# Optimization experiments

Measured on AMD Instinct MI355X. Metric: run time of the kernel, lower is better.

The kernel has to match this reference:

```python
import jax, jax.numpy as jnp
import numpy as np

B, N, K, H = 8, 2048, 30, 128
SCALE = 30.0
EPS = 1e-5


def _gelu(x):
    return jax.nn.gelu(x, approximate=False)


def _lin(x, w, b):
    return x @ w.T + b


def _ln(x, g, b):
    m = x.mean(-1, keepdims=True)
    v = ((x - m) ** 2).mean(-1, keepdims=True)
    return g * (x - m) * jax.lax.rsqrt(v + EPS) + b


def _gather_nodes(h_V, E_idx):
    # h_V: [B,N,H], E_idx: [B,N,K] -> [B,N,K,H]
    b_idx = jnp.arange(h_V.shape[0])[:, None, None]
    return h_V[b_idx, E_idx]


def setup_inputs() -> dict:
    key = jax.random.key(0)
    ks = jax.random.split(key, 16)
    p = 0.02
    inp = {
        'h_V': jax.random.normal(ks[0], (B, N, H), jnp.float32),
        'h_E': jax.random.normal(ks[1], (B, N, K, H), jnp.float32),
        'E_idx': jax.random.randint(ks[2], (B, N, K), 0, N, jnp.int32),
        'mask_V': jnp.ones((B, N), jnp.float32),
        'mask_attend': jnp.ones((B, N, K), jnp.float32),
        # node message MLP (3H -> H -> H -> H)
        'W1_w': jax.random.normal(ks[3], (H, 3 * H), jnp.float32) * p,
        'W1_b': jnp.zeros((H,), jnp.float32),
        'W2_w': jax.random.normal(ks[4], (H, H), jnp.float32) * p,
        'W2_b': jnp.zeros((H,), jnp.float32),
        'W3_w': jax.random.normal(ks[5], (H, H), jnp.float32) * p,
        'W3_b': jnp.zeros((H,), jnp.float32),
        # edge message MLP (3H -> H -> H -> H)
        'W11_w': jax.random.normal(ks[6], (H, 3 * H), jnp.float32) * p,
        'W11_b': jnp.zeros((H,), jnp.float32),
        'W12_w': jax.random.normal(ks[7], (H, H), jnp.float32) * p,
        'W12_b': jnp.zeros((H,), jnp.float32),
        'W13_w': jax.random.normal(ks[8], (H, H), jnp.float32) * p,
        'W13_b': jnp.zeros((H,), jnp.float32),
        # layer norms
        'n1_g': jnp.ones((H,), jnp.float32), 'n1_b': jnp.zeros((H,), jnp.float32),
        'n2_g': jnp.ones((H,), jnp.float32), 'n2_b': jnp.zeros((H,), jnp.float32),
        'n3_g': jnp.ones((H,), jnp.float32), 'n3_b': jnp.zeros((H,), jnp.float32),
        # position-wise FFN (H -> 4H -> H)
        'din_w': jax.random.normal(ks[9], (4 * H, H), jnp.float32) * p,
        'din_b': jnp.zeros((4 * H,), jnp.float32),
        'dout_w': jax.random.normal(ks[10], (H, 4 * H), jnp.float32) * p,
        'dout_b': jnp.zeros((H,), jnp.float32),
    }
    return inp


def reference(h_V, h_E, E_idx, mask_V, mask_attend,
              W1_w, W1_b, W2_w, W2_b, W3_w, W3_b,
              W11_w, W11_b, W12_w, W12_b, W13_w, W13_b,
              n1_g, n1_b, n2_g, n2_b, n3_g, n3_b,
              din_w, din_b, dout_w, dout_b):
    k = h_E.shape[-2]
    # --- node update ---
    h_nbr = _gather_nodes(h_V, E_idx)                       # [B,N,K,H]
    h_V_exp = jnp.broadcast_to(h_V[:, :, None, :], h_nbr.shape)
    h_EV = jnp.concatenate([h_V_exp, h_nbr, h_E], axis=-1)  # [B,N,K,3H]
    h_message = _lin(_gelu(_lin(_gelu(_lin(h_EV, W1_w, W1_b)), W2_w, W2_b)), W3_w, W3_b)
    h_message = mask_attend[..., None] * h_message
    dh = jnp.sum(h_message, axis=-2) / SCALE
    h_V = _ln(h_V + dh, n1_g, n1_b)
    dh = _lin(_gelu(_lin(h_V, din_w, din_b)), dout_w, dout_b)
    h_V = _ln(h_V + dh, n2_g, n2_b)
    h_V = mask_V[..., None] * h_V
    # --- edge update ---
    h_nbr = _gather_nodes(h_V, E_idx)
    h_V_exp = jnp.broadcast_to(h_V[:, :, None, :], h_nbr.shape)
    h_EV = jnp.concatenate([h_V_exp, h_nbr, h_E], axis=-1)
    h_message = _lin(_gelu(_lin(_gelu(_lin(h_EV, W11_w, W11_b)), W12_w, W12_b)), W13_w, W13_b)
    h_E = _ln(h_E + h_message, n3_g, n3_b)
    return (h_V, h_E)
```

## Files before the change

### kernel.cpp

```cpp
#include <hip/hip_runtime.h>

#define B_ 8
#define N_ 2048
#define K_ 30
#define H_ 128
#define LDA 136
#define EPS_ 1e-5f

typedef __attribute__((ext_vector_type(8))) short short8;
typedef __attribute__((ext_vector_type(4))) float f32x4;

__device__ inline unsigned pkbf(float lo, float hi) {
  unsigned r;
  asm("v_cvt_pk_bf16_f32 %0, %1, %2" : "=v"(r) : "v"(lo), "v"(hi));
  return r;
}

__device__ inline unsigned short f2bf(float f) { return (unsigned short)pkbf(f, f); }

__device__ inline float bf2f(unsigned short h) {
  union { unsigned u; float f; } v; v.u = ((unsigned)h) << 16; return v.f;
}

__device__ inline float gelu_t(float x) {
  const float p = x * x;
  const float z = x * (1.5957691216057308f + 0.07135481627f * p);
  const float e = exp2f(z * -1.4426950408889634f);
  return x * __builtin_amdgcn_rcpf(1.0f + e);
}

__device__ inline short8 pack8(float4 a, float4 b) {
  union { unsigned u[4]; short8 s; } v;
  v.u[0] = pkbf(a.x, a.y); v.u[1] = pkbf(a.z, a.w);
  v.u[2] = pkbf(b.x, b.y); v.u[3] = pkbf(b.z, b.w);
  return v.s;
}

template<int LDW>
__device__ inline void gemmT(const unsigned short* __restrict__ sA,
                             const unsigned short* __restrict__ W,
                             int lane, int cb, f32x4 (&acc)[4][2]) {
  const int rl = lane & 15;
  const int klo = (lane >> 4) << 3;
#pragma unroll
  for (int ks = 0; ks < 4; ++ks) {
    short8 wf[2];
#pragma unroll
    for (int fn = 0; fn < 2; ++fn)
      wf[fn] = *(const short8*)(W + (size_t)(cb + fn * 16 + rl) * LDW + ks * 32 + klo);
#pragma unroll
    for (int et = 0; et < 4; ++et) {
      const short8 ef = *(const short8*)(sA + (et * 16 + rl) * LDA + ks * 32 + klo);
      acc[et][0] = __builtin_amdgcn_mfma_f32_16x16x32_bf16(wf[0], ef, acc[et][0], 0, 0, 0);
      acc[et][1] = __builtin_amdgcn_mfma_f32_16x16x32_bf16(wf[1], ef, acc[et][1], 0, 0, 0);
    }
  }
}

#define ZERO42(A) \
  _Pragma("unroll") for (int e_ = 0; e_ < 4; ++e_) { A[e_][0] = (f32x4){0,0,0,0}; A[e_][1] = (f32x4){0,0,0,0}; }

template<int LDW, int NN>
__device__ inline void gemm64(const unsigned short* __restrict__ sA,
                              const unsigned short* __restrict__ W,
                              int lane, int cb, f32x4 (&acc)[4][NN]) {
  const int rl = lane & 15;
  const int klo = (lane >> 4) << 3;
#pragma unroll
  for (int ks = 0; ks < 4; ++ks) {
    short8 a[4];
#pragma unroll
    for (int m = 0; m < 4; ++m)
      a[m] = *(const short8*)(sA + (m * 16 + rl) * LDA + ks * 32 + klo);
#pragma unroll
    for (int n = 0; n < NN; ++n) {
      const short8 b8 = *(const short8*)(W + (size_t)(cb + n * 16 + rl) * LDW + ks * 32 + klo);
#pragma unroll
      for (int m = 0; m < 4; ++m)
        acc[m][n] = __builtin_amdgcn_mfma_f32_16x16x32_bf16(a[m], b8, acc[m][n], 0, 0, 0);
    }
  }
}

__global__ __launch_bounds__(256) void prep(const float* __restrict__ w1, const float* __restrict__ w2,
                                            const float* __restrict__ w3, const float* __restrict__ w11,
                                            const float* __restrict__ w12, const float* __restrict__ w13,
                                            const float* __restrict__ din, const float* __restrict__ dout,
                                            unsigned short* __restrict__ dst) {
  const int i = blockIdx.x * 256 + threadIdx.x;
  const float* s; int off;
  if (i < 49152)       { s = w1;  off = 0; }
  else if (i < 65536)  { s = w2;  off = 49152; }
  else if (i < 81920)  { s = w3;  off = 65536; }
  else if (i < 131072) { s = w11; off = 81920; }
  else if (i < 147456) { s = w12; off = 131072; }
  else if (i < 163840) { s = w13; off = 147456; }
  else if (i < 229376) { s = din; off = 163840; }
  else                 { s = dout; off = 229376; }
  dst[i] = f2bf(s[i - off]);
}

template<bool F32SRC, bool SPLIT>
__global__ __launch_bounds__(256) void preY(const void* __restrict__ Xv,
                                            const unsigned short* __restrict__ Wbase,
                                            unsigned short* __restrict__ Yc,
                                            unsigned short* __restrict__ Yn) {
  __shared__ __align__(16) unsigned short sA[64 * LDA];
  const int tid = threadIdx.x;
  const int lane = tid & 63;
  const int w = tid >> 6;
  const int rows = blockIdx.x << 6;
  const int rl = lane & 15;
  const int h4 = (lane >> 4) << 2;

  if (F32SRC) {
    const float* X = (const float*)Xv;
    for (int t = tid; t < 1024; t += 256) {
      const int r = t >> 4, seg = t & 15;
      const float* src = X + (((size_t)(rows + r)) << 7) + seg * 8;
      *(short8*)(sA + r * LDA + seg * 8) = pack8(*(const float4*)src, *(const float4*)(src + 4));
    }
  } else {
    const unsigned short* X = (const unsigned short*)Xv;
    for (int t = tid; t < 1024; t += 256) {
      const int r = t >> 4, seg = t & 15;
      *(short8*)(sA + r * LDA + seg * 8) =
          *(const short8*)(X + (((size_t)(rows + r)) << 7) + seg * 8);
    }
  }
  __syncthreads();

  const int half = w >> 1;
  const int cb = (w & 1) * 64;
  f32x4 acc[4][4];
#pragma unroll
  for (int m = 0; m < 4; ++m)
#pragma unroll
    for (int n = 0; n < 4; ++n) acc[m][n] = (f32x4){0, 0, 0, 0};
  gemm64<384, 4>(sA, Wbase + half * 128, lane, cb, acc);

  unsigned short* Y = half ? Yn : Yc;
  const int stride = SPLIT ? 128 : 256;
  const int coff = SPLIT ? 0 : half * 128;
#pragma unroll
  for (int n = 0; n < 4; ++n) {
    const int col = coff + cb + n * 16 + rl;
#pragma unroll
    for (int m = 0; m < 4; ++m)
#pragma unroll
      for (int i = 0; i < 4; ++i)
        Y[(size_t)(rows + m * 16 + h4 + i) * stride + col] = f2bf(acc[m][n][i]);
  }
}

__global__ __launch_bounds__(256, 6) void k1(
    const float* __restrict__ hV, const float* __restrict__ hE,
    const int* __restrict__ Eidx, const float* __restrict__ mattend,
    const unsigned short* __restrict__ wc, const unsigned short* __restrict__ Y1,
    const float* __restrict__ W1b, const float* __restrict__ W2b,
    const float* __restrict__ W3b, const float* __restrict__ n1g,
    const float* __restrict__ n1b, unsigned short* __restrict__ hV1b) {
  __shared__ __align__(16) unsigned short sA[64 * LDA];
  __shared__ __align__(16) unsigned short sYc[2 * 128];
  __shared__ float sMask[64];
  __shared__ float sRed[2][128];

  const int tid = threadIdx.x;
  const int lane = tid & 63;
  const int w = tid >> 6;
  const int rl = lane & 15;
  const int h4 = (lane >> 4) << 2;
  const int bid = (blockIdx.x & 7) * 1024 + (blockIdx.x >> 3);
  const int v0 = bid << 1;
  const int b = v0 >> 11;
  const int n0 = v0 & (N_ - 1);
  const int bBase = b * N_;

  const unsigned short* W1c = wc;
  const unsigned short* W2c = wc + 49152;
  const unsigned short* W3c = wc + 65536;

  for (int t = tid; t < 1024; t += 256) {
    const int r = t >> 4, seg = t & 15;
    const int g = r >> 5;
    int kk = r & 31; if (kk >= K_) kk = K_ - 1;
    const size_t e = (size_t)(bBase + n0 + g) * K_ + kk;
    const float* src = hE + (e << 7) + seg * 8;
    *(short8*)(sA + r * LDA + seg * 8) = pack8(*(const float4*)src, *(const float4*)(src + 4));
  }
  {
    const int g = tid >> 7, c = tid & 127;
    sYc[g * 128 + c] = Y1[(size_t)(bBase + n0 + g) * 256 + c];
  }
  if (tid < 64) {
    const int g = tid >> 5, kk = tid & 31;
    sMask[tid] = (kk < K_) ? mattend[(bBase + n0 + g) * K_ + kk] : 0.f;
  }
  __syncthreads();

  f32x4 acc[4][2];
  ZERO42(acc)
  gemmT<384>(sA, W1c + 256, lane, w * 32, acc);
  __syncthreads();

  for (int t = tid; t < 1024; t += 256) {
    const int r = t >> 4, seg = t & 15;
    const int g = r >> 5;
    int kk = r & 31; if (kk >= K_) kk = K_ - 1;
    const int j = Eidx[(bBase + n0 + g) * K_ + kk];
    *(short8*)(sA + r * LDA + seg * 8) =
        *(const short8*)(Y1 + (size_t)(bBase + j) * 256 + 128 + seg * 8);
  }
  __syncthreads();

  {
    float4 b1v[2];
    b1v[0] = *(const float4*)(W1b + w * 32 + h4);
    b1v[1] = *(const float4*)(W1b + w * 32 + 16 + h4);
#pragma unroll
    for (int et = 0; et < 4; ++et) {
      const int e = et * 16 + rl;
      const int g = et >> 1;
#pragma unroll
      for (int fn = 0; fn < 2; ++fn) {
        const int f0 = w * 32 + fn * 16 + h4;
        const ushort4 yc = *(const ushort4*)(sYc + g * 128 + f0);
        const ushort4 yn = *(const ushort4*)(sA + e * LDA + f0);
        const float x0 = gelu_t(acc[et][fn][0] + b1v[fn].x + bf2f(yc.x) + bf2f(yn.x));
        const float x1 = gelu_t(acc[et][fn][1] + b1v[fn].y + bf2f(yc.y) + bf2f(yn.y));
        const float x2 = gelu_t(acc[et][fn][2] + b1v[fn].z + bf2f(yc.z) + bf2f(yn.z));
        const float x3 = gelu_t(acc[et][fn][3] + b1v[fn].w + bf2f(yc.w) + bf2f(yn.w));
        uint2 o; o.x = pkbf(x0, x1); o.y = pkbf(x2, x3);
        *(uint2*)(sA + e * LDA + f0) = o;
      }
    }
  }
  __syncthreads();

  f32x4 acc2[4][2];
  ZERO42(acc2)
  gemmT<128>(sA, W2c, lane, w * 32, acc2);
  __syncthreads();
  {
    float4 b2v[2];
    b2v[0] = *(const float4*)(W2b + w * 32 + h4);
    b2v[1] = *(const float4*)(W2b + w * 32 + 16 + h4);
#pragma unroll
    for (int et = 0; et < 4; ++et) {
      const int e = et * 16 + rl;
#pragma unroll
      for (int fn = 0; fn < 2; ++fn) {
        const int f0 = w * 32 + fn * 16 + h4;
        const float x0 = gelu_t(acc2[et][fn][0] + b2v[fn].x);
        const float x1 = gelu_t(acc2[et][fn][1] + b2v[fn].y);
        const float x2 = gelu_t(acc2[et][fn][2] + b2v[fn].z);
        const float x3 = gelu_t(acc2[et][fn][3] + b2v[fn].w);
        uint2 o; o.x = pkbf(x0, x1); o.y = pkbf(x2, x3);
        *(uint2*)(sA + e * LDA + f0) = o;
      }
    }
  }
  __syncthreads();

  f32x4 acc3[4][2];
  ZERO42(acc3)
  gemmT<128>(sA, W3c, lane, w * 32, acc3);
  __syncthreads();

  {
    float4 b3v[2];
    b3v[0] = *(const float4*)(W3b + w * 32 + h4);
    b3v[1] = *(const float4*)(W3b + w * 32 + 16 + h4);
#pragma unroll
    for (int et = 0; et < 4; ++et) {
      const int e = et * 16 + rl;
      const float mk = sMask[e];
#pragma unroll
      for (int fn = 0; fn < 2; ++fn) {
        const int f0 = w * 32 + fn * 16 + h4;
        uint2 o;
        o.x = pkbf((acc3[et][fn][0] + b3v[fn].x) * mk, (acc3[et][fn][1] + b3v[fn].y) * mk);
        o.y = pkbf((acc3[et][fn][2] + b3v[fn].z) * mk, (acc3[et][fn][3] + b3v[fn].w) * mk);
        *(uint2*)(sA + e * LDA + f0) = o;
      }
    }
  }
  __syncthreads();

  {
    const int g = tid >> 7, f = tid & 127;
    float s = 0.f;
#pragma unroll
    for (int kk = 0; kk < 32; ++kk) s += bf2f(sA[(g * 32 + kk) * LDA + f]);
    sRed[g][f] = s;
  }
  __syncthreads();

  if (w < 2) {
    const size_t base = ((size_t)(bBase + n0 + w)) << 7;
    const float x0 = hV[base + lane] + sRed[w][lane] * (1.0f / 30.0f);
    const float x1 = hV[base + 64 + lane] + sRed[w][64 + lane] * (1.0f / 30.0f);
    float s = x0 + x1;
#pragma unroll
    for (int o = 1; o < 64; o <<= 1) s += __shfl_xor(s, o);
    const float mean = s * (1.0f / 128.0f);
    const float d0 = x0 - mean, d1 = x1 - mean;
    float vs = d0 * d0 + d1 * d1;
#pragma unroll
    for (int o = 1; o < 64; o <<= 1) vs += __shfl_xor(vs, o);
    const float inv = rsqrtf(vs * (1.0f / 128.0f) + EPS_);
    hV1b[base + lane] = f2bf(n1g[lane] * (d0 * inv) + n1b[lane]);
    hV1b[base + 64 + lane] = f2bf(n1g[64 + lane] * (d1 * inv) + n1b[64 + lane]);
  }
}

__global__ __launch_bounds__(256) void k2(
    const unsigned short* __restrict__ hV1b, const unsigned short* __restrict__ wc,
    const float* __restrict__ dinb, const float* __restrict__ doutb,
    const float* __restrict__ n2g, const float* __restrict__ n2b,
    const float* __restrict__ maskV, float* __restrict__ outV,
    unsigned short* __restrict__ hV2c) {
  __shared__ __align__(16) unsigned short sT[16 * LDA];
  __shared__ float sStat[16][2][4];

  const int tid = threadIdx.x;
  const int lane = tid & 63;
  const int w = tid >> 6;
  const int rl = lane & 15;
  const int h4 = (lane >> 4) << 2;
  const int klo = (lane >> 4) << 3;
  const int rowbase = blockIdx.x << 4;

  const unsigned short* dinc = wc + 163840;
  const unsigned short* doutc = wc + 229376;

  short8 ef[4];
#pragma unroll
  for (int ks = 0; ks < 4; ++ks)
    ef[ks] = *(const short8*)(hV1b + (((size_t)(rowbase + rl)) << 7) + ks * 32 + klo);

  f32x4 acc2[2];
  acc2[0] = (f32x4){0, 0, 0, 0}; acc2[1] = (f32x4){0, 0, 0, 0};

  for (int c = 0; c < 4; ++c) {
    f32x4 acc1[2];
    acc1[0] = (f32x4){0, 0, 0, 0}; acc1[1] = (f32x4){0, 0, 0, 0};
#pragma unroll
    for (int ks = 0; ks < 4; ++ks)
#pragma unroll
      for (int fn = 0; fn < 2; ++fn) {
        const short8 wf = *(const short8*)(dinc + (size_t)(c * 128 + w * 32 + fn * 16 + rl) * 128 + ks * 32 + klo);
        acc1[fn] = __builtin_amdgcn_mfma_f32_16x16x32_bf16(wf, ef[ks], acc1[fn], 0, 0, 0);
      }
    __syncthreads();
    {
      float4 db[2];
      db[0] = *(const float4*)(dinb + c * 128 + w * 32 + h4);
      db[1] = *(const float4*)(dinb + c * 128 + w * 32 + 16 + h4);
#pragma unroll
      for (int fn = 0; fn < 2; ++fn) {
        const int f0 = w * 32 + fn * 16 + h4;
        const float x0 = gelu_t(acc1[fn][0] + db[fn].x);
        const float x1 = gelu_t(acc1[fn][1] + db[fn].y);
        const float x2 = gelu_t(acc1[fn][2] + db[fn].z);
        const float x3 = gelu_t(acc1[fn][3] + db[fn].w);
        uint2 o; o.x = pkbf(x0, x1); o.y = pkbf(x2, x3);
        *(uint2*)(sT + rl * LDA + f0) = o;
      }
    }
    __syncthreads();
#pragma unroll
    for (int ks = 0; ks < 4; ++ks) {
      const short8 xf = *(const short8*)(sT + rl * LDA + ks * 32 + klo);
#pragma unroll
      for (int fn = 0; fn < 2; ++fn) {
        const short8 wf2 = *(const short8*)(doutc + (size_t)(w * 32 + fn * 16 + rl) * 512 + c * 128 + ks * 32 + klo);
        acc2[fn] = __builtin_amdgcn_mfma_f32_16x16x32_bf16(wf2, xf, acc2[fn], 0, 0, 0);
      }
    }
  }

  const int row = rl;
  const int grow = rowbase + row;
  {
    float4 wbv[2];
    wbv[0] = *(const float4*)(doutb + w * 32 + h4);
    wbv[1] = *(const float4*)(doutb + w * 32 + 16 + h4);
    float s = 0.f, ss = 0.f;
#pragma unroll
    for (int fn = 0; fn < 2; ++fn) {
      const int f0 = w * 32 + fn * 16 + h4;
      const ushort4 rr = *(const ushort4*)(hV1b + (((size_t)grow) << 7) + f0);
      const float x0 = acc2[fn][0] + wbv[fn].x + bf2f(rr.x);
      const float x1 = acc2[fn][1] + wbv[fn].y + bf2f(rr.y);
      const float x2 = acc2[fn][2] + wbv[fn].z + bf2f(rr.z);
      const float x3 = acc2[fn][3] + wbv[fn].w + bf2f(rr.w);
      acc2[fn] = (f32x4){x0, x1, x2, x3};
      s += x0 + x1 + x2 + x3;
      ss += x0 * x0 + x1 * x1 + x2 * x2 + x3 * x3;
    }
    s += __shfl_xor(s, 16); s += __shfl_xor(s, 32);
    ss += __shfl_xor(ss, 16); ss += __shfl_xor(ss, 32);
    if (lane < 16) { sStat[row][0][w] = s; sStat[row][1][w] = ss; }
  }
  __syncthreads();
  {
    const float sum = sStat[row][0][0] + sStat[row][0][1] + sStat[row][0][2] + sStat[row][0][3];
    const float ssq = sStat[row][1][0] + sStat[row][1][1] + sStat[row][1][2] + sStat[row][1][3];
    const float mean = sum * (1.0f / 128.0f);
    const float inv = rsqrtf(ssq * (1.0f / 128.0f) - mean * mean + EPS_);
    const float mv = maskV[grow];
#pragma unroll
    for (int fn = 0; fn < 2; ++fn) {
      const int f0 = w * 32 + fn * 16 + h4;
      const float4 gv = *(const float4*)(n2g + f0);
      const float4 bv = *(const float4*)(n2b + f0);
      const float y0 = (gv.x * (acc2[fn][0] - mean) * inv + bv.x) * mv;
      const float y1 = (gv.y * (acc2[fn][1] - mean) * inv + bv.y) * mv;
      const float y2 = (gv.z * (acc2[fn][2] - mean) * inv + bv.z) * mv;
      const float y3 = (gv.w * (acc2[fn][3] - mean) * inv + bv.w) * mv;
      *(float4*)(outV + (((size_t)grow) << 7) + f0) = make_float4(y0, y1, y2, y3);
      uint2 o; o.x = pkbf(y0, y1); o.y = pkbf(y2, y3);
      *(uint2*)(hV2c + (((size_t)grow) << 7) + f0) = o;
    }
  }
}

__global__ __launch_bounds__(256, 6) void k3(
    const float* __restrict__ hE, const int* __restrict__ Eidx,
    const unsigned short* __restrict__ wc,
    const unsigned short* __restrict__ Y2c, const unsigned short* __restrict__ Y2n,
    const float* __restrict__ W11b, const float* __restrict__ W12b,
    const float* __restrict__ W13b, const float* __restrict__ n3g,
    const float* __restrict__ n3b, float* __restrict__ outE) {
  __shared__ __align__(16) unsigned short sA[64 * LDA];
  __shared__ unsigned short sYc[2 * 128];
  __shared__ float sStat[64][2][4];

  const int tid = threadIdx.x;
  const int lane = tid & 63;
  const int w = tid >> 6;
  const int rl = lane & 15;
  const int h4 = (lane >> 4) << 2;
  const int bid = (blockIdx.x & 7) * 1024 + (blockIdx.x >> 3);
  const int v0 = bid << 1;
  const int b = v0 >> 11;
  const int n0 = v0 & (N_ - 1);
  const int bBase = b * N_;

  const unsigned short* W11c = wc + 81920;
  const unsigned short* W12c = wc + 131072;
  const unsigned short* W13c = wc + 147456;

  for (int t = tid; t < 1024; t += 256) {
    const int r = t >> 4, seg = t & 15;
    const int g = r >> 5;
    int kk = r & 31; if (kk >= K_) kk = K_ - 1;
    const size_t e = (size_t)(bBase + n0 + g) * K_ + kk;
    const float* src = hE + (e << 7) + seg * 8;
    *(short8*)(sA + r * LDA + seg * 8) = pack8(*(const float4*)src, *(const float4*)(src + 4));
  }
  {
    const int g = tid >> 7, c = tid & 127;
    sYc[g * 128 + c] = Y2c[(size_t)(bBase + n0 + g) * 128 + c];
  }
  __syncthreads();

  f32x4 acc[4][2];
  ZERO42(acc)
  gemm64<384, 2>(sA, W11c + 256, lane, w * 32, acc);
  __syncthreads();

  for (int t = tid; t < 1024; t += 256) {
    const int r = t >> 4, seg = t & 15;
    const int g = r >> 5;
    int kk = r & 31; if (kk >= K_) kk = K_ - 1;
    const int j = Eidx[(bBase + n0 + g) * K_ + kk];
    *(short8*)(sA + r * LDA + seg * 8) =
        *(const short8*)(Y2n + (size_t)(bBase + j) * 128 + seg * 8);
  }
  __syncthreads();

#pragma unroll
  for (int n = 0; n < 2; ++n) {
    const int f = w * 32 + n * 16 + rl;
    const float bb = W11b[f];
#pragma unroll
    for (int m = 0; m < 4; ++m)
#pragma unroll
      for (int i = 0; i < 4; ++i) {
        const int e = m * 16 + h4 + i;
        const float x = acc[m][n][i] + bb + bf2f(sYc[(e >> 5) * 128 + f]) + bf2f(sA[e * LDA + f]);
        sA[e * LDA + f] = f2bf(gelu_t(x));
      }
  }
  __syncthreads();

  f32x4 acc2[4][2];
  ZERO42(acc2)
  gemm64<128, 2>(sA, W12c, lane, w * 32, acc2);
  __syncthreads();
#pragma unroll
  for (int n = 0; n < 2; ++n) {
    const int f = w * 32 + n * 16 + rl;
    const float bb = W12b[f];
#pragma unroll
    for (int m = 0; m < 4; ++m)
#pragma unroll
      for (int i = 0; i < 4; ++i) {
        const int e = m * 16 + h4 + i;
        sA[e * LDA + f] = f2bf(gelu_t(acc2[m][n][i] + bb));
      }
  }
  __syncthreads();

  f32x4 acc3[4][2];
  ZERO42(acc3)
  gemm64<128, 2>(sA, W13c, lane, w * 32, acc3);

  float gc[2], bc[2], wb[2];
#pragma unroll
  for (int n = 0; n < 2; ++n) {
    const int f = w * 32 + n * 16 + rl;
    gc[n] = n3g[f]; bc[n] = n3b[f]; wb[n] = W13b[f];
  }
#pragma unroll
  for (int m = 0; m < 4; ++m)
#pragma unroll
    for (int i = 0; i < 4; ++i) {
      const int e = m * 16 + h4 + i;
      const int g = e >> 5, kk = e & 31;
      const bool valid = kk < K_;
      const float* er = hE + (((size_t)((bBase + n0 + g) * K_ + (valid ? kk : K_ - 1))) << 7) + w * 32 + rl;
      float s = 0.f, ss = 0.f;
#pragma unroll
      for (int n = 0; n < 2; ++n) {
        float x = acc3[m][n][i] + wb[n];
        if (valid) x += er[n * 16];
        acc3[m][n][i] = x;
        s += x; ss += x * x;
      }
#pragma unroll
      for (int o = 1; o <= 8; o <<= 1) { s += __shfl_xor(s, o); ss += __shfl_xor(ss, o); }
      if (rl == 0) { sStat[e][0][w] = s; sStat[e][1][w] = ss; }
    }
  __syncthreads();
#pragma unroll
  for (int m = 0; m < 4; ++m)
#pragma unroll
    for (int i = 0; i < 4; ++i) {
      const int e = m * 16 + h4 + i;
      const int g = e >> 5, kk = e & 31;
      if (kk >= K_) continue;
      const float sum = sStat[e][0][0] + sStat[e][0][1] + sStat[e][0][2] + sStat[e][0][3];
      const float ssq = sStat[e][1][0] + sStat[e][1][1] + sStat[e][1][2] + sStat[e][1][3];
      const float mean = sum * (1.0f / 128.0f);
      const float inv = rsqrtf(ssq * (1.0f / 128.0f) - mean * mean + EPS_);
      float* dst = outE + (((size_t)((bBase + n0 + g) * K_ + kk)) << 7) + w * 32 + rl;
#pragma unroll
      for (int n = 0; n < 2; ++n)
        dst[n * 16] = gc[n] * (acc3[m][n][i] - mean) * inv + bc[n];
    }
}

extern "C" void kernel_launch(void* const* d_in, const int* in_sizes, int n_in,
                              void* d_out, int out_size, void* d_ws, size_t ws_size,
                              hipStream_t stream) {
  const float* hV = (const float*)d_in[0];
  const float* hE = (const float*)d_in[1];
  const int* Eidx = (const int*)d_in[2];
  const float* maskV = (const float*)d_in[3];
  const float* mattend = (const float*)d_in[4];
  const float* W1w = (const float*)d_in[5];   const float* W1b = (const float*)d_in[6];
  const float* W2w = (const float*)d_in[7];   const float* W2b = (const float*)d_in[8];
  const float* W3w = (const float*)d_in[9];   const float* W3b = (const float*)d_in[10];
  const float* W11w = (const float*)d_in[11]; const float* W11b = (const float*)d_in[12];
  const float* W12w = (const float*)d_in[13]; const float* W12b = (const float*)d_in[14];
  const float* W13w = (const float*)d_in[15]; const float* W13b = (const float*)d_in[16];
  const float* n1g = (const float*)d_in[17];  const float* n1b = (const float*)d_in[18];
  const float* n2g = (const float*)d_in[19];  const float* n2b = (const float*)d_in[20];
  const float* n3g = (const float*)d_in[21];  const float* n3b = (const float*)d_in[22];
  const float* dinw = (const float*)d_in[23]; const float* dinb = (const float*)d_in[24];
  const float* doutw = (const float*)d_in[25]; const float* doutb = (const float*)d_in[26];

  unsigned short* wc   = (unsigned short*)d_ws;
  unsigned short* R1   = wc + 294912;
  unsigned short* R2   = R1 + 4194304;
  unsigned short* Y1   = R1;
  unsigned short* hV1b = R2;
  unsigned short* hV2c = R1;
  unsigned short* Y2c  = R1 + 2097152;
  unsigned short* Y2n  = R2;

  float* outV = (float*)d_out;
  float* outE = outV + (size_t)B_ * N_ * H_;

  prep<<<1152, 256, 0, stream>>>(W1w, W2w, W3w, W11w, W12w, W13w, dinw, doutw, wc);
  preY<true, false><<<256, 256, 0, stream>>>(hV, wc, Y1, Y1);
  k1<<<8192, 256, 0, stream>>>(hV, hE, Eidx, mattend, wc, Y1,
                               W1b, W2b, W3b, n1g, n1b, hV1b);
  k2<<<1024, 256, 0, stream>>>(hV1b, wc, dinb, doutb, n2g, n2b, maskV, outV, hV2c);
  preY<false, true><<<256, 256, 0, stream>>>(hV2c, wc + 81920, Y2c, Y2n);
  k3<<<8192, 256, 0, stream>>>(hE, Eidx, wc, Y2c, Y2n,
                               W11b, W12b, W13b, n3g, n3b, outE);
}
```

Measured before the change: 479.0 us.

## Stash bf16 copy of h_E in output buffer during k1 and reuse in k3

k1 now writes a bf16-packed copy of each h_E row into the upper half of that row's fp32 slot in the edge output buffer. k3 reads this bf16 copy instead of re-reading fp32 h_E, both for the GEMM input tile and for the residual add before the layer norm. The aim is to roughly halve k3's h_E read traffic, at the cost of extra writes in k1. The residual add now uses a bf16-rounded h_E instead of fp32, which lowers precision. Launch bounds for k1 and k3 also drop from 6 to 4 blocks per CU.

```diff
diff --git a/kernel.cpp b/kernel.cpp
--- a/kernel.cpp
+++ b/kernel.cpp
@@ -153,13 +153,14 @@
   }
 }
 
-__global__ __launch_bounds__(256, 6) void k1(
+__global__ __launch_bounds__(256, 4) void k1(
     const float* __restrict__ hV, const float* __restrict__ hE,
     const int* __restrict__ Eidx, const float* __restrict__ mattend,
     const unsigned short* __restrict__ wc, const unsigned short* __restrict__ Y1,
     const float* __restrict__ W1b, const float* __restrict__ W2b,
     const float* __restrict__ W3b, const float* __restrict__ n1g,
-    const float* __restrict__ n1b, unsigned short* __restrict__ hV1b) {
+    const float* __restrict__ n1b, unsigned short* __restrict__ hV1b,
+    float* __restrict__ outE) {
   __shared__ __align__(16) unsigned short sA[64 * LDA];
   __shared__ __align__(16) unsigned short sYc[2 * 128];
   __shared__ float sMask[64];
@@ -182,11 +183,14 @@
 
   for (int t = tid; t < 1024; t += 256) {
     const int r = t >> 4, seg = t & 15;
-    const int g = r >> 5;
-    int kk = r & 31; if (kk >= K_) kk = K_ - 1;
-    const size_t e = (size_t)(bBase + n0 + g) * K_ + kk;
+    const int g = r >> 5, kk = r & 31;
+    const int kc = kk < K_ ? kk : K_ - 1;
+    const size_t e = (size_t)(bBase + n0 + g) * K_ + kc;
     const float* src = hE + (e << 7) + seg * 8;
-    *(short8*)(sA + r * LDA + seg * 8) = pack8(*(const float4*)src, *(const float4*)(src + 4));
+    const short8 o = pack8(*(const float4*)src, *(const float4*)(src + 4));
+    *(short8*)(sA + r * LDA + seg * 8) = o;
+    if (kk < K_)
+      *(short8*)((unsigned short*)(outE + (e << 7)) + 128 + seg * 8) = o;
   }
   {
     const int g = tid >> 7, c = tid & 127;
@@ -426,9 +430,8 @@
   }
 }
 
-__global__ __launch_bounds__(256, 6) void k3(
-    const float* __restrict__ hE, const int* __restrict__ Eidx,
-    const unsigned short* __restrict__ wc,
+__global__ __launch_bounds__(256, 4) void k3(
+    const int* __restrict__ Eidx, const unsigned short* __restrict__ wc,
     const unsigned short* __restrict__ Y2c, const unsigned short* __restrict__ Y2n,
     const float* __restrict__ W11b, const float* __restrict__ W12b,
     const float* __restrict__ W13b, const float* __restrict__ n3g,
@@ -457,8 +460,8 @@
     const int g = r >> 5;
     int kk = r & 31; if (kk >= K_) kk = K_ - 1;
     const size_t e = (size_t)(bBase + n0 + g) * K_ + kk;
-    const float* src = hE + (e << 7) + seg * 8;
-    *(short8*)(sA + r * LDA + seg * 8) = pack8(*(const float4*)src, *(const float4*)(src + 4));
+    *(short8*)(sA + r * LDA + seg * 8) =
+        *(const short8*)((const unsigned short*)(outE + (e << 7)) + 128 + seg * 8);
   }
   {
     const int g = tid >> 7, c = tid & 127;
@@ -531,12 +534,14 @@
       const int e = m * 16 + h4 + i;
       const int g = e >> 5, kk = e & 31;
       const bool valid = kk < K_;
-      const float* er = hE + (((size_t)((bBase + n0 + g) * K_ + (valid ? kk : K_ - 1))) << 7) + w * 32 + rl;
+      const size_t erow = (size_t)((bBase + n0 + g) * K_ + (valid ? kk : K_ - 1));
+      const unsigned short* er =
+          (const unsigned short*)(outE + (erow << 7)) + 128 + w * 32 + rl;
       float s = 0.f, ss = 0.f;
 #pragma unroll
       for (int n = 0; n < 2; ++n) {
         float x = acc3[m][n][i] + wb[n];
-        if (valid) x += er[n * 16];
+        if (valid) x += bf2f(er[n * 16]);
         acc3[m][n][i] = x;
         s += x; ss += x * x;
       }
@@ -598,9 +603,9 @@
   prep<<<1152, 256, 0, stream>>>(W1w, W2w, W3w, W11w, W12w, W13w, dinw, doutw, wc);
   preY<true, false><<<256, 256, 0, stream>>>(hV, wc, Y1, Y1);
   k1<<<8192, 256, 0, stream>>>(hV, hE, Eidx, mattend, wc, Y1,
-                               W1b, W2b, W3b, n1g, n1b, hV1b);
+                               W1b, W2b, W3b, n1g, n1b, hV1b, outE);
   k2<<<1024, 256, 0, stream>>>(hV1b, wc, dinb, doutb, n2g, n2b, maskV, outV, hV2c);
   preY<false, true><<<256, 256, 0, stream>>>(hV2c, wc + 81920, Y2c, Y2n);
-  k3<<<8192, 256, 0, stream>>>(hE, Eidx, wc, Y2c, Y2n,
+  k3<<<8192, 256, 0, stream>>>(Eidx, wc, Y2c, Y2n,
                                W11b, W12b, W13b, n3g, n3b, outE);
 }
```

After: 492.1 us. 1.03x slower.
